# Performance work log

Measured on AMD Instinct MI355X. Metric: run time of the kernel, lower is better.

Reference implementation:

```python
import jax, jax.numpy as jnp
import numpy as np

# Key observation: the TF module groups ROIs per image (boolean_mask), runs the
# same MLP on each group, concatenates the ragged results, then argsort-gathers
# to restore the ORIGINAL row order. Since the Dense/ReLU MLP acts row-wise and
# identically for every image, the group -> MLP -> regroup pipeline is exactly
# equivalent to applying the MLP to all rows in their original order. The clean
# JAX reference therefore computes the same math with a single fused GEMM chain.

NUM_CLASSES = 81
HIDDEN_DIM = 1024
N = 2048          # total ROIs
SS = 7            # sample_size
FS = 256          # feature_size
FEAT_DIM = SS * SS * FS  # 12544
NUM_IMAGES = 8


def setup_inputs() -> dict:
    key = jax.random.key(0)
    ks = jax.random.split(key, 8)
    features = jax.random.normal(ks[0], (N, SS, SS, FS), dtype=jnp.float32)
    batch_indices = jnp.sort(jax.random.randint(ks[1], (N,), 0, NUM_IMAGES, dtype=jnp.int32))
    s1 = 1.0 / np.sqrt(FEAT_DIM)
    s2 = 1.0 / np.sqrt(HIDDEN_DIM)
    W1 = jax.random.uniform(ks[2], (FEAT_DIM, HIDDEN_DIM), jnp.float32, -s1, s1)
    b1 = jnp.zeros((HIDDEN_DIM,), jnp.float32)
    W2 = jax.random.uniform(ks[3], (HIDDEN_DIM, HIDDEN_DIM), jnp.float32, -s2, s2)
    b2 = jnp.zeros((HIDDEN_DIM,), jnp.float32)
    Wc = jax.random.uniform(ks[4], (HIDDEN_DIM, NUM_CLASSES), jnp.float32, -s2, s2)
    bc = jnp.zeros((NUM_CLASSES,), jnp.float32)
    return {"features": features, "batch_indices": batch_indices,
            "W1": W1, "b1": b1, "W2": W2, "b2": b2, "Wc": Wc, "bc": bc}


def reference(features, batch_indices, W1, b1, W2, b2, Wc, bc):
    # Group/ungroup in the original is an identity permutation on rows, but we
    # reproduce it explicitly and cheaply: stable-sort rows by image id, run the
    # MLP, then invert the permutation via argsort (same as TF argsort-gather).
    order = jnp.argsort(batch_indices, stable=True)          # group rows per image
    x = features[order].reshape(features.shape[0], -1)       # [N, feat_dim]
    x = jax.nn.relu(x @ W1 + b1)
    x = jax.nn.relu(x @ W2 + b2)
    logits = x @ Wc + bc                                     # [N, num_classes]
    inv = jnp.argsort(order)                                 # restore original order
    return logits[inv]
```

## Files before the change

kernel.cpp:

```cpp
#include <hip/hip_runtime.h>
#include <hip/hip_bf16.h>
#include <stdint.h>

typedef __bf16 bf16_t;
typedef __bf16 bf16x4 __attribute__((ext_vector_type(4)));
typedef __bf16 bf16x8 __attribute__((ext_vector_type(8)));
typedef float f32x4 __attribute__((ext_vector_type(4)));

__device__ __forceinline__ void async_ld16(const bf16_t* g, bf16_t* lds) {
    __builtin_amdgcn_global_load_lds(
        (__attribute__((address_space(1))) void*)g,
        (__attribute__((address_space(3))) void*)lds,
        16, 0, 0);
}


__device__ __forceinline__ void transpose_tile(
    const float* __restrict__ in, bf16_t* __restrict__ out,
    int R, int C, int Cp, int tileIdx, int tid, float (*tile)[33])
{
    const int tilesX = Cp / 32;
    const int c0 = (tileIdx % tilesX) * 32;
    const int r0 = (tileIdx / tilesX) * 32;
    const int tx = tid & 31;
    const int ty = tid >> 5;
#pragma unroll
    for (int i = 0; i < 32; i += 8) {
        int rr = r0 + ty + i, cc = c0 + tx;
        float v = 0.f;
        if (cc < C) v = in[(size_t)rr * C + cc];
        tile[ty + i][tx] = v;
    }
    __syncthreads();
#pragma unroll
    for (int i = 0; i < 32; i += 8) {
        int oc = c0 + ty + i;
        int orr = r0 + tx;
        out[(size_t)oc * R + orr] = (bf16_t)tile[tx][ty + i];
    }
}

__global__ void prep_all(const float* __restrict__ X, bf16_t* __restrict__ Xb, int n4,
                         const float* __restrict__ W1, bf16_t* __restrict__ W1T,
                         const float* __restrict__ W2, bf16_t* __restrict__ W2T,
                         const float* __restrict__ Wc, bf16_t* __restrict__ WcT,
                         int FEAT, int HID, int NC, int NCP,
                         int nCvt, int t1, int t2)
{
    __shared__ float tile[32][33];
    int bid = blockIdx.x;
    int tid = threadIdx.x;
    if (bid < nCvt) {
        int i = bid * 256 + tid;
        if (i < n4) {
            float4 v = ((const float4*)X)[i];
            bf16x4 o = { (bf16_t)v.x, (bf16_t)v.y, (bf16_t)v.z, (bf16_t)v.w };
            ((bf16x4*)Xb)[i] = o;
        }
        return;
    }
    bid -= nCvt;
    if (bid < t1) { transpose_tile(W1, W1T, FEAT, HID, HID, bid, tid, tile); return; }
    bid -= t1;
    if (bid < t2) { transpose_tile(W2, W2T, HID, HID, HID, bid, tid, tile); return; }
    bid -= t2;
    transpose_tile(Wc, WcT, HID, NC, NCP, bid, tid, tile);
}

__global__ __launch_bounds__(256) void gemm128_splitk(
    const bf16_t* __restrict__ A, const bf16_t* __restrict__ B,
    float* __restrict__ P, int M, int N, int K, int KC)
{
    __shared__ __align__(16) bf16_t Asm[128 * 32];
    __shared__ __align__(16) bf16_t Bsm[128 * 32];

    const int tid  = threadIdx.x;
    const int wave = tid >> 6;
    const int lane = tid & 63;
    const int bm = blockIdx.x, bn = blockIdx.y, s = blockIdx.z;

    const bf16_t* Ab = A + (size_t)bm * 128 * K + (size_t)s * KC;
    const bf16_t* Bb = B + (size_t)bn * 128 * K + (size_t)s * KC;

    const int ar = lane >> 2;
    const int ak = (((lane & 3) ^ ((ar >> 1) & 3))) * 8;

    const int wm = (wave >> 1) * 64;
    const int wn = (wave & 1) * 64;
    const int r  = lane & 15;
    const int physc = (((lane >> 4) ^ ((r >> 1) & 3))) * 8;

    f32x4 acc[4][4];
#pragma unroll
    for (int i = 0; i < 4; ++i)
#pragma unroll
        for (int j = 0; j < 4; ++j)
            acc[i][j] = f32x4{0.f, 0.f, 0.f, 0.f};

    for (int k0 = 0; k0 < KC; k0 += 32) {
        __syncthreads();
#pragma unroll
        for (int i = 0; i < 2; ++i) {
            const int rb = (wave * 2 + i) * 16;
            async_ld16(Ab + (size_t)(rb + ar) * K + (k0 + ak), &Asm[rb * 32]);
            async_ld16(Bb + (size_t)(rb + ar) * K + (k0 + ak), &Bsm[rb * 32]);
        }
        __syncthreads();

        bf16x8 af[4], bfr[4];
#pragma unroll
        for (int i = 0; i < 4; ++i)
            af[i] = *(const bf16x8*)&Asm[(wm + i * 16 + r) * 32 + physc];
#pragma unroll
        for (int j = 0; j < 4; ++j)
            bfr[j] = *(const bf16x8*)&Bsm[(wn + j * 16 + r) * 32 + physc];
#pragma unroll
        for (int i = 0; i < 4; ++i)
#pragma unroll
            for (int j = 0; j < 4; ++j)
                acc[i][j] = __builtin_amdgcn_mfma_f32_16x16x32_bf16(af[i], bfr[j], acc[i][j], 0, 0, 0);
    }

    float* Pb = P + ((size_t)s * M + (size_t)bm * 128) * N + (size_t)bn * 128;
    const int r4 = (lane >> 4) * 4;
    const int c  = lane & 15;
#pragma unroll
    for (int i = 0; i < 4; ++i)
#pragma unroll
        for (int j = 0; j < 4; ++j)
#pragma unroll
            for (int rg = 0; rg < 4; ++rg)
                Pb[(size_t)(wm + i * 16 + r4 + rg) * N + (wn + j * 16 + c)] = acc[i][j][rg];
}

template <bool RELU, typename OutT>
__global__ __launch_bounds__(256) void gemm64_fused(
    const bf16_t* __restrict__ A, const bf16_t* __restrict__ B,
    const float* __restrict__ bias, OutT* __restrict__ out,
    int K, int Nout)
{
    __shared__ __align__(16) bf16_t Asm[64 * 64];
    __shared__ __align__(16) bf16_t Bsm[64 * 64];

    const int tid  = threadIdx.x;
    const int wave = tid >> 6;
    const int lane = tid & 63;
    const int bm = blockIdx.x, bn = blockIdx.y;

    const bf16_t* Ab = A + (size_t)bm * 64 * K;
    const bf16_t* Bb = B + (size_t)bn * 64 * K;

    const int sr = lane >> 3;
    const int sk = ((lane & 7) ^ (sr & 7)) * 8;

    const int wm = (wave >> 1) * 32;
    const int wn = (wave & 1) * 32;
    const int r  = lane & 15;
    const int q  = lane >> 4;

    f32x4 acc[2][2];
#pragma unroll
    for (int i = 0; i < 2; ++i)
#pragma unroll
        for (int j = 0; j < 2; ++j)
            acc[i][j] = f32x4{0.f, 0.f, 0.f, 0.f};

    for (int k0 = 0; k0 < K; k0 += 64) {
        __syncthreads();
#pragma unroll
        for (int i = 0; i < 2; ++i) {
            const int rb = wave * 16 + i * 8;
            async_ld16(Ab + (size_t)(rb + sr) * K + (k0 + sk), &Asm[rb * 64]);
            async_ld16(Bb + (size_t)(rb + sr) * K + (k0 + sk), &Bsm[rb * 64]);
        }
        __syncthreads();

#pragma unroll
        for (int rnd = 0; rnd < 2; ++rnd) {
            bf16x8 af[2], bfr[2];
#pragma unroll
            for (int i = 0; i < 2; ++i)
                af[i] = *(const bf16x8*)&Asm[(wm + i * 16 + r) * 64
                                             + ((rnd * 4 + q) ^ (r & 7)) * 8];
#pragma unroll
            for (int j = 0; j < 2; ++j)
                bfr[j] = *(const bf16x8*)&Bsm[(wn + j * 16 + r) * 64
                                              + ((rnd * 4 + q) ^ (r & 7)) * 8];
#pragma unroll
            for (int i = 0; i < 2; ++i)
#pragma unroll
                for (int j = 0; j < 2; ++j)
                    acc[i][j] = __builtin_amdgcn_mfma_f32_16x16x32_bf16(af[i], bfr[j], acc[i][j], 0, 0, 0);
        }
    }

    const int r4 = (lane >> 4) * 4;
    const int c  = lane & 15;
#pragma unroll
    for (int i = 0; i < 2; ++i)
#pragma unroll
        for (int j = 0; j < 2; ++j) {
            const int col = bn * 64 + wn + j * 16 + c;
            if (col < Nout) {
                const float bv = bias[col];
#pragma unroll
                for (int rg = 0; rg < 4; ++rg) {
                    const int row = bm * 64 + wm + i * 16 + r4 + rg;
                    float v = acc[i][j][rg] + bv;
                    if (RELU) v = fmaxf(v, 0.f);
                    out[(size_t)row * Nout + col] = (OutT)v;
                }
            }
        }
}


template <int S>
__global__ void reduce_relu_bf16_k(const float* __restrict__ P, const float* __restrict__ bias,
                                   bf16_t* __restrict__ h, int MN, int Nm1) {
    int i4 = (blockIdx.x * 256 + threadIdx.x) * 4;
    if (i4 >= MN) return;
    int n = i4 & Nm1;
    float4 a = *(const float4*)(bias + n);
#pragma unroll
    for (int s = 0; s < S; ++s) {
        float4 p = *(const float4*)(P + (size_t)s * MN + i4);
        a.x += p.x; a.y += p.y; a.z += p.z; a.w += p.w;
    }
    a.x = fmaxf(a.x, 0.f); a.y = fmaxf(a.y, 0.f);
    a.z = fmaxf(a.z, 0.f); a.w = fmaxf(a.w, 0.f);
    bf16x4 o = { (bf16_t)a.x, (bf16_t)a.y, (bf16_t)a.z, (bf16_t)a.w };
    *(bf16x4*)(h + i4) = o;
}


extern "C" void kernel_launch(void* const* d_in, const int* in_sizes, int n_in,
                              void* d_out, int out_size, void* d_ws, size_t ws_size,
                              hipStream_t stream) {
    const float* X  = (const float*)d_in[0];
    const float* W1 = (const float*)d_in[2];
    const float* b1 = (const float*)d_in[3];
    const float* W2 = (const float*)d_in[4];
    const float* b2 = (const float*)d_in[5];
    const float* Wc = (const float*)d_in[6];
    const float* bc = (const float*)d_in[7];
    float* out = (float*)d_out;

    const int M    = in_sizes[1];
    const int FEAT = in_sizes[0] / M;
    const int HID  = in_sizes[3];
    const int NC   = in_sizes[7];
    const int NCP  = 128;

    char* ws = (char*)d_ws;
    size_t off = 0;
    auto alloc = [&](size_t bytes) {
        char* p = ws + off;
        off += (bytes + 255) & ~(size_t)255;
        return p;
    };
    bf16_t* Xb  = (bf16_t*)alloc((size_t)M * FEAT * 2);
    bf16_t* W1T = (bf16_t*)alloc((size_t)FEAT * HID * 2);
    bf16_t* W2T = (bf16_t*)alloc((size_t)HID * HID * 2);
    bf16_t* WcT = (bf16_t*)alloc((size_t)NCP * HID * 2);
    bf16_t* h1  = (bf16_t*)alloc((size_t)M * HID * 2);
    bf16_t* h2  = (bf16_t*)alloc((size_t)M * HID * 2);
    float*  P   = (float*)(ws + off);

    size_t rem  = ws_size > off ? ws_size - off : 0;
    size_t perS = (size_t)M * HID * 4;
    int S1 = (rem >= 8 * perS) ? 8 : (rem >= 4 * perS) ? 4 : (rem >= 2 * perS) ? 2 : 1;
    int KC1 = ((FEAT / S1 + 31) / 32) * 32;

    int n4   = (M * FEAT) / 4;
    int nCvt = (n4 + 255) / 256;
    int t1 = (HID / 32) * (FEAT / 32);
    int t2 = (HID / 32) * (HID / 32);
    int t3 = (NCP / 32) * (HID / 32);
    prep_all<<<nCvt + t1 + t2 + t3, 256, 0, stream>>>(
        X, Xb, n4, W1, W1T, W2, W2T, Wc, WcT, FEAT, HID, NC, NCP, nCvt, t1, t2);

    gemm128_splitk<<<dim3(M / 128, HID / 128, S1), 256, 0, stream>>>(Xb, W1T, P, M, HID, FEAT, KC1);
    switch (S1) {
        case 8: reduce_relu_bf16_k<8><<<(M * HID / 4 + 255) / 256, 256, 0, stream>>>(P, b1, h1, M * HID, HID - 1); break;
        case 4: reduce_relu_bf16_k<4><<<(M * HID / 4 + 255) / 256, 256, 0, stream>>>(P, b1, h1, M * HID, HID - 1); break;
        case 2: reduce_relu_bf16_k<2><<<(M * HID / 4 + 255) / 256, 256, 0, stream>>>(P, b1, h1, M * HID, HID - 1); break;
        default: reduce_relu_bf16_k<1><<<(M * HID / 4 + 255) / 256, 256, 0, stream>>>(P, b1, h1, M * HID, HID - 1); break;
    }

    gemm64_fused<true, bf16_t><<<dim3(M / 64, HID / 64), 256, 0, stream>>>(h1, W2T, b2, h2, HID, HID);

    gemm64_fused<false, float><<<dim3(M / 64, NCP / 64), 256, 0, stream>>>(h2, WcT, bc, out, HID, NC);
}
```

Measured before the change: 316.7 us.

## Fuse fp32-to-bf16 activation conversion into first GEMM with double-buffered LDS

Removes the separate pass that converts the fp32 feature matrix to bf16 in workspace. The first split-K GEMM now reads fp32 activations directly, converts them in registers, and stores them into swizzled LDS. It also switches from async global-to-LDS loads to register-staged double buffering, so the next tile's global loads overlap the current MFMA step. The cost is twice as many bytes of A read from global memory per GEMM tile, repeated across the N-blocks, plus higher register pressure. Also KC1 is no longer rounded to a multiple of 32.

```diff
diff --git a/kernel.cpp b/kernel.cpp
--- a/kernel.cpp
+++ b/kernel.cpp
@@ -40,26 +40,14 @@
     }
 }
 
-__global__ void prep_all(const float* __restrict__ X, bf16_t* __restrict__ Xb, int n4,
-                         const float* __restrict__ W1, bf16_t* __restrict__ W1T,
-                         const float* __restrict__ W2, bf16_t* __restrict__ W2T,
-                         const float* __restrict__ Wc, bf16_t* __restrict__ WcT,
-                         int FEAT, int HID, int NC, int NCP,
-                         int nCvt, int t1, int t2)
+__global__ void prep_weights(const float* __restrict__ W1, bf16_t* __restrict__ W1T,
+                             const float* __restrict__ W2, bf16_t* __restrict__ W2T,
+                             const float* __restrict__ Wc, bf16_t* __restrict__ WcT,
+                             int FEAT, int HID, int NC, int NCP, int t1, int t2)
 {
     __shared__ float tile[32][33];
     int bid = blockIdx.x;
     int tid = threadIdx.x;
-    if (bid < nCvt) {
-        int i = bid * 256 + tid;
-        if (i < n4) {
-            float4 v = ((const float4*)X)[i];
-            bf16x4 o = { (bf16_t)v.x, (bf16_t)v.y, (bf16_t)v.z, (bf16_t)v.w };
-            ((bf16x4*)Xb)[i] = o;
-        }
-        return;
-    }
-    bid -= nCvt;
     if (bid < t1) { transpose_tile(W1, W1T, FEAT, HID, HID, bid, tid, tile); return; }
     bid -= t1;
     if (bid < t2) { transpose_tile(W2, W2T, HID, HID, HID, bid, tid, tile); return; }
@@ -67,28 +55,34 @@
     transpose_tile(Wc, WcT, HID, NC, NCP, bid, tid, tile);
 }
 
-__global__ __launch_bounds__(256) void gemm128_splitk(
-    const bf16_t* __restrict__ A, const bf16_t* __restrict__ B,
+__global__ __launch_bounds__(256) void gemm128_pipe(
+    const float* __restrict__ A, const bf16_t* __restrict__ B,
     float* __restrict__ P, int M, int N, int K, int KC)
 {
-    __shared__ __align__(16) bf16_t Asm[128 * 32];
-    __shared__ __align__(16) bf16_t Bsm[128 * 32];
+    __shared__ __align__(16) bf16_t Asm[2][128 * 32];
+    __shared__ __align__(16) bf16_t Bsm[2][128 * 32];
 
     const int tid  = threadIdx.x;
     const int wave = tid >> 6;
     const int lane = tid & 63;
     const int bm = blockIdx.x, bn = blockIdx.y, s = blockIdx.z;
 
-    const bf16_t* Ab = A + (size_t)bm * 128 * K + (size_t)s * KC;
-    const bf16_t* Bb = B + (size_t)bn * 128 * K + (size_t)s * KC;
-
-    const int ar = lane >> 2;
-    const int ak = (((lane & 3) ^ ((ar >> 1) & 3))) * 8;
+    const float*  Ag = A + (size_t)bm * 128 * K + (size_t)s * KC;
+    const bf16_t* Bg = B + (size_t)bn * 128 * K + (size_t)s * KC;
+
+    const int srow = tid >> 1;
+    const int skh  = (tid & 1) * 16;
+    const float*  Ar = Ag + (size_t)srow * K + skh;
+    const bf16_t* Br = Bg + (size_t)srow * K + skh;
+    const int swz = (srow >> 1) & 3;
+    const int c0  = skh >> 3;
+    const int wo0 = srow * 32 + ((c0 ^ swz)) * 8;
+    const int wo1 = srow * 32 + (((c0 + 1) ^ swz)) * 8;
 
     const int wm = (wave >> 1) * 64;
     const int wn = (wave & 1) * 64;
     const int r  = lane & 15;
-    const int physc = (((lane >> 4) ^ ((r >> 1) & 3))) * 8;
+    const int physc = ((lane >> 4) ^ ((r >> 1) & 3)) * 8;
 
     f32x4 acc[4][4];
 #pragma unroll
@@ -97,29 +91,57 @@
         for (int j = 0; j < 4; ++j)
             acc[i][j] = f32x4{0.f, 0.f, 0.f, 0.f};
 
-    for (int k0 = 0; k0 < KC; k0 += 32) {
-        __syncthreads();
-#pragma unroll
-        for (int i = 0; i < 2; ++i) {
-            const int rb = (wave * 2 + i) * 16;
-            async_ld16(Ab + (size_t)(rb + ar) * K + (k0 + ak), &Asm[rb * 32]);
-            async_ld16(Bb + (size_t)(rb + ar) * K + (k0 + ak), &Bsm[rb * 32]);
-        }
-        __syncthreads();
-
+    float4 a0, a1, a2, a3;
+    bf16x8 b0, b1;
+
+    auto loads = [&](int k0) {
+        const float* ap = Ar + k0;
+        a0 = *(const float4*)(ap + 0);
+        a1 = *(const float4*)(ap + 4);
+        a2 = *(const float4*)(ap + 8);
+        a3 = *(const float4*)(ap + 12);
+        const bf16x8* bp = (const bf16x8*)(Br + k0);
+        b0 = bp[0];
+        b1 = bp[1];
+    };
+    auto commit = [&](int buf) {
+        bf16x8 va, vb;
+        va[0] = (bf16_t)a0.x; va[1] = (bf16_t)a0.y; va[2] = (bf16_t)a0.z; va[3] = (bf16_t)a0.w;
+        va[4] = (bf16_t)a1.x; va[5] = (bf16_t)a1.y; va[6] = (bf16_t)a1.z; va[7] = (bf16_t)a1.w;
+        vb[0] = (bf16_t)a2.x; vb[1] = (bf16_t)a2.y; vb[2] = (bf16_t)a2.z; vb[3] = (bf16_t)a2.w;
+        vb[4] = (bf16_t)a3.x; vb[5] = (bf16_t)a3.y; vb[6] = (bf16_t)a3.z; vb[7] = (bf16_t)a3.w;
+        *(bf16x8*)&Asm[buf][wo0] = va;
+        *(bf16x8*)&Asm[buf][wo1] = vb;
+        *(bf16x8*)&Bsm[buf][wo0] = b0;
+        *(bf16x8*)&Bsm[buf][wo1] = b1;
+    };
+    auto mfma_step = [&](int buf) {
         bf16x8 af[4], bfr[4];
 #pragma unroll
         for (int i = 0; i < 4; ++i)
-            af[i] = *(const bf16x8*)&Asm[(wm + i * 16 + r) * 32 + physc];
+            af[i] = *(const bf16x8*)&Asm[buf][(wm + i * 16 + r) * 32 + physc];
 #pragma unroll
         for (int j = 0; j < 4; ++j)
-            bfr[j] = *(const bf16x8*)&Bsm[(wn + j * 16 + r) * 32 + physc];
+            bfr[j] = *(const bf16x8*)&Bsm[buf][(wn + j * 16 + r) * 32 + physc];
 #pragma unroll
         for (int i = 0; i < 4; ++i)
 #pragma unroll
             for (int j = 0; j < 4; ++j)
                 acc[i][j] = __builtin_amdgcn_mfma_f32_16x16x32_bf16(af[i], bfr[j], acc[i][j], 0, 0, 0);
-    }
+    };
+
+    loads(0);
+    commit(0);
+    __syncthreads();
+    int cur = 0;
+    for (int k0 = 32; k0 < KC; k0 += 32) {
+        loads(k0);
+        mfma_step(cur);
+        commit(cur ^ 1);
+        __syncthreads();
+        cur ^= 1;
+    }
+    mfma_step(cur);
 
     float* Pb = P + ((size_t)s * M + (size_t)bm * 128) * N + (size_t)bn * 128;
     const int r4 = (lane >> 4) * 4;
@@ -259,7 +281,6 @@
         off += (bytes + 255) & ~(size_t)255;
         return p;
     };
-    bf16_t* Xb  = (bf16_t*)alloc((size_t)M * FEAT * 2);
     bf16_t* W1T = (bf16_t*)alloc((size_t)FEAT * HID * 2);
     bf16_t* W2T = (bf16_t*)alloc((size_t)HID * HID * 2);
     bf16_t* WcT = (bf16_t*)alloc((size_t)NCP * HID * 2);
@@ -270,17 +291,15 @@
     size_t rem  = ws_size > off ? ws_size - off : 0;
     size_t perS = (size_t)M * HID * 4;
     int S1 = (rem >= 8 * perS) ? 8 : (rem >= 4 * perS) ? 4 : (rem >= 2 * perS) ? 2 : 1;
-    int KC1 = ((FEAT / S1 + 31) / 32) * 32;
-
-    int n4   = (M * FEAT) / 4;
-    int nCvt = (n4 + 255) / 256;
+    int KC1 = FEAT / S1;
+
     int t1 = (HID / 32) * (FEAT / 32);
     int t2 = (HID / 32) * (HID / 32);
     int t3 = (NCP / 32) * (HID / 32);
-    prep_all<<<nCvt + t1 + t2 + t3, 256, 0, stream>>>(
-        X, Xb, n4, W1, W1T, W2, W2T, Wc, WcT, FEAT, HID, NC, NCP, nCvt, t1, t2);
-
-    gemm128_splitk<<<dim3(M / 128, HID / 128, S1), 256, 0, stream>>>(Xb, W1T, P, M, HID, FEAT, KC1);
+    prep_weights<<<t1 + t2 + t3, 256, 0, stream>>>(
+        W1, W1T, W2, W2T, Wc, WcT, FEAT, HID, NC, NCP, t1, t2);
+
+    gemm128_pipe<<<dim3(M / 128, HID / 128, S1), 256, 0, stream>>>(X, W1T, P, M, HID, FEAT, KC1);
     switch (S1) {
         case 8: reduce_relu_bf16_k<8><<<(M * HID / 4 + 255) / 256, 256, 0, stream>>>(P, b1, h1, M * HID, HID - 1); break;
         case 4: reduce_relu_bf16_k<4><<<(M * HID / 4 + 255) / 256, 256, 0, stream>>>(P, b1, h1, M * HID, HID - 1); break;
```

Result: slower. 357.4 us (+12.9%).

## Fuse fp32-to-bf16 activation conversion into the first GEMM's LDS load path

Applied to the files above, without the earlier changes.

The separate pass that converted the whole fp32 feature matrix to bf16 is removed. The first split-K GEMM now streams fp32 activations straight into LDS with async loads and converts them to bf16 while building MFMA fragments, using a new XOR swizzle for the fp32 tile. This saves a full write and re-read of the 2048x12544 activation buffer. In exchange, A-tile global traffic and LDS use double, and every block that shares an M tile repeats the conversion work. The weight transpose also writes paired bf16 values to widen its stores.

```diff
diff --git a/kernel.cpp b/kernel.cpp
--- a/kernel.cpp
+++ b/kernel.cpp
@@ -3,11 +3,13 @@
 #include <stdint.h>
 
 typedef __bf16 bf16_t;
+typedef __bf16 bf16x2 __attribute__((ext_vector_type(2)));
 typedef __bf16 bf16x4 __attribute__((ext_vector_type(4)));
 typedef __bf16 bf16x8 __attribute__((ext_vector_type(8)));
 typedef float f32x4 __attribute__((ext_vector_type(4)));
 
-__device__ __forceinline__ void async_ld16(const bf16_t* g, bf16_t* lds) {
+template <typename T>
+__device__ __forceinline__ void async_ld16(const T* g, T* lds) {
     __builtin_amdgcn_global_load_lds(
         (__attribute__((address_space(1))) void*)g,
         (__attribute__((address_space(3))) void*)lds,
@@ -32,34 +34,25 @@
         tile[ty + i][tx] = v;
     }
     __syncthreads();
-#pragma unroll
-    for (int i = 0; i < 32; i += 8) {
-        int oc = c0 + ty + i;
-        int orr = r0 + tx;
-        out[(size_t)oc * R + orr] = (bf16_t)tile[tx][ty + i];
-    }
-}
-
-__global__ void prep_all(const float* __restrict__ X, bf16_t* __restrict__ Xb, int n4,
-                         const float* __restrict__ W1, bf16_t* __restrict__ W1T,
-                         const float* __restrict__ W2, bf16_t* __restrict__ W2T,
-                         const float* __restrict__ Wc, bf16_t* __restrict__ WcT,
-                         int FEAT, int HID, int NC, int NCP,
-                         int nCvt, int t1, int t2)
+    const int px = tid & 15;
+    const int py = tid >> 4;
+#pragma unroll
+    for (int i = 0; i < 32; i += 16) {
+        int oc = c0 + py + i;
+        int orr = r0 + px * 2;
+        bf16x2 o = { (bf16_t)tile[px * 2][py + i], (bf16_t)tile[px * 2 + 1][py + i] };
+        *(bf16x2*)&out[(size_t)oc * R + orr] = o;
+    }
+}
+
+__global__ void prep_weights(const float* __restrict__ W1, bf16_t* __restrict__ W1T,
+                             const float* __restrict__ W2, bf16_t* __restrict__ W2T,
+                             const float* __restrict__ Wc, bf16_t* __restrict__ WcT,
+                             int FEAT, int HID, int NC, int NCP, int t1, int t2)
 {
     __shared__ float tile[32][33];
     int bid = blockIdx.x;
     int tid = threadIdx.x;
-    if (bid < nCvt) {
-        int i = bid * 256 + tid;
-        if (i < n4) {
-            float4 v = ((const float4*)X)[i];
-            bf16x4 o = { (bf16_t)v.x, (bf16_t)v.y, (bf16_t)v.z, (bf16_t)v.w };
-            ((bf16x4*)Xb)[i] = o;
-        }
-        return;
-    }
-    bid -= nCvt;
     if (bid < t1) { transpose_tile(W1, W1T, FEAT, HID, HID, bid, tid, tile); return; }
     bid -= t1;
     if (bid < t2) { transpose_tile(W2, W2T, HID, HID, HID, bid, tid, tile); return; }
@@ -67,11 +60,11 @@
     transpose_tile(Wc, WcT, HID, NC, NCP, bid, tid, tile);
 }
 
-__global__ __launch_bounds__(256) void gemm128_splitk(
-    const bf16_t* __restrict__ A, const bf16_t* __restrict__ B,
+__global__ __launch_bounds__(256) void gemm128_xf32(
+    const float* __restrict__ A, const bf16_t* __restrict__ B,
     float* __restrict__ P, int M, int N, int K, int KC)
 {
-    __shared__ __align__(16) bf16_t Asm[128 * 32];
+    __shared__ __align__(16) float  Asm[128 * 32];
     __shared__ __align__(16) bf16_t Bsm[128 * 32];
 
     const int tid  = threadIdx.x;
@@ -79,16 +72,21 @@
     const int lane = tid & 63;
     const int bm = blockIdx.x, bn = blockIdx.y, s = blockIdx.z;
 
-    const bf16_t* Ab = A + (size_t)bm * 128 * K + (size_t)s * KC;
+    const float*  Ab = A + (size_t)bm * 128 * K + (size_t)s * KC;
     const bf16_t* Bb = B + (size_t)bn * 128 * K + (size_t)s * KC;
 
-    const int ar = lane >> 2;
-    const int ak = (((lane & 3) ^ ((ar >> 1) & 3))) * 8;
+    const int arow = lane >> 3;
+    const int akf  = ((lane & 7) ^ arow) * 4;
+    const int brow = lane >> 2;
+    const int bke  = ((lane & 3) ^ ((brow >> 1) & 3)) * 8;
 
     const int wm = (wave >> 1) * 64;
     const int wn = (wave & 1) * 64;
     const int r  = lane & 15;
-    const int physc = (((lane >> 4) ^ ((r >> 1) & 3))) * 8;
+    const int q  = lane >> 4;
+    const int physB = (q ^ ((r >> 1) & 3)) * 8;
+    const int pA0 = ((2 * q) ^ (r & 7)) * 4;
+    const int pA1 = ((2 * q + 1) ^ (r & 7)) * 4;
 
     f32x4 acc[4][4];
 #pragma unroll
@@ -100,20 +98,31 @@
     for (int k0 = 0; k0 < KC; k0 += 32) {
         __syncthreads();
 #pragma unroll
+        for (int i = 0; i < 4; ++i) {
+            const int rb = wave * 32 + i * 8;
+            async_ld16(Ab + (size_t)(rb + arow) * K + (k0 + akf), &Asm[rb * 32]);
+        }
+#pragma unroll
         for (int i = 0; i < 2; ++i) {
             const int rb = (wave * 2 + i) * 16;
-            async_ld16(Ab + (size_t)(rb + ar) * K + (k0 + ak), &Asm[rb * 32]);
-            async_ld16(Bb + (size_t)(rb + ar) * K + (k0 + ak), &Bsm[rb * 32]);
+            async_ld16(Bb + (size_t)(rb + brow) * K + (k0 + bke), &Bsm[rb * 32]);
         }
         __syncthreads();
 
         bf16x8 af[4], bfr[4];
 #pragma unroll
-        for (int i = 0; i < 4; ++i)
-            af[i] = *(const bf16x8*)&Asm[(wm + i * 16 + r) * 32 + physc];
+        for (int i = 0; i < 4; ++i) {
+            const int rr = (wm + i * 16 + r) * 32;
+            f32x4 lo = *(const f32x4*)&Asm[rr + pA0];
+            f32x4 hi = *(const f32x4*)&Asm[rr + pA1];
+            af[i][0] = (bf16_t)lo[0]; af[i][1] = (bf16_t)lo[1];
+            af[i][2] = (bf16_t)lo[2]; af[i][3] = (bf16_t)lo[3];
+            af[i][4] = (bf16_t)hi[0]; af[i][5] = (bf16_t)hi[1];
+            af[i][6] = (bf16_t)hi[2]; af[i][7] = (bf16_t)hi[3];
+        }
 #pragma unroll
         for (int j = 0; j < 4; ++j)
-            bfr[j] = *(const bf16x8*)&Bsm[(wn + j * 16 + r) * 32 + physc];
+            bfr[j] = *(const bf16x8*)&Bsm[(wn + j * 16 + r) * 32 + physB];
 #pragma unroll
         for (int i = 0; i < 4; ++i)
 #pragma unroll
@@ -122,8 +131,8 @@
     }
 
     float* Pb = P + ((size_t)s * M + (size_t)bm * 128) * N + (size_t)bn * 128;
-    const int r4 = (lane >> 4) * 4;
-    const int c  = lane & 15;
+    const int r4 = q * 4;
+    const int c  = r;
 #pragma unroll
     for (int i = 0; i < 4; ++i)
 #pragma unroll
@@ -259,7 +268,6 @@
         off += (bytes + 255) & ~(size_t)255;
         return p;
     };
-    bf16_t* Xb  = (bf16_t*)alloc((size_t)M * FEAT * 2);
     bf16_t* W1T = (bf16_t*)alloc((size_t)FEAT * HID * 2);
     bf16_t* W2T = (bf16_t*)alloc((size_t)HID * HID * 2);
     bf16_t* WcT = (bf16_t*)alloc((size_t)NCP * HID * 2);
@@ -270,17 +278,15 @@
     size_t rem  = ws_size > off ? ws_size - off : 0;
     size_t perS = (size_t)M * HID * 4;
     int S1 = (rem >= 8 * perS) ? 8 : (rem >= 4 * perS) ? 4 : (rem >= 2 * perS) ? 2 : 1;
-    int KC1 = ((FEAT / S1 + 31) / 32) * 32;
-
-    int n4   = (M * FEAT) / 4;
-    int nCvt = (n4 + 255) / 256;
+    int KC1 = FEAT / S1;
+
     int t1 = (HID / 32) * (FEAT / 32);
     int t2 = (HID / 32) * (HID / 32);
     int t3 = (NCP / 32) * (HID / 32);
-    prep_all<<<nCvt + t1 + t2 + t3, 256, 0, stream>>>(
-        X, Xb, n4, W1, W1T, W2, W2T, Wc, WcT, FEAT, HID, NC, NCP, nCvt, t1, t2);
-
-    gemm128_splitk<<<dim3(M / 128, HID / 128, S1), 256, 0, stream>>>(Xb, W1T, P, M, HID, FEAT, KC1);
+    prep_weights<<<t1 + t2 + t3, 256, 0, stream>>>(
+        W1, W1T, W2, W2T, Wc, WcT, FEAT, HID, NC, NCP, t1, t2);
+
+    gemm128_xf32<<<dim3(M / 128, HID / 128, S1), 256, 0, stream>>>(X, W1T, P, M, HID, FEAT, KC1);
     switch (S1) {
         case 8: reduce_relu_bf16_k<8><<<(M * HID / 4 + 255) / 256, 256, 0, stream>>>(P, b1, h1, M * HID, HID - 1); break;
         case 4: reduce_relu_bf16_k<4><<<(M * HID / 4 + 255) / 256, 256, 0, stream>>>(P, b1, h1, M * HID, HID - 1); break;
```

New measurement: 364.9 us. 1.15x slower.
